# Kernel optimization log

Hardware: AMD Instinct MI355X
Metric: run time of the kernel (lower is better)

The kernel has to match this reference:

```python
import jax, jax.numpy as jnp
import numpy as np

BETA = 0.25  # commitment weight per level (vqconfig default)
EPS = 1e-12  # F.normalize eps


def setup_inputs() -> dict:
    key = jax.random.key(0)
    k1, k2 = jax.random.split(key)
    z = jax.random.normal(k1, (4, 256, 32, 32), dtype=jnp.float32)
    cb = jax.random.normal(k2, (4, 4096, 256), dtype=jnp.float32)
    # embeddings are row-normalized at init in the torch module
    cb = cb / jnp.maximum(jnp.linalg.norm(cb, axis=-1, keepdims=True), EPS)
    return {"z": z, "codebooks": cb}


def _nearest_code(r_flat, embed):
    """use_znorm=True path: cosine-similarity nearest neighbor.
    r_flat: (N, C), embed: (K, C) -> idx: (N,) int32"""
    rn = r_flat / jnp.maximum(jnp.linalg.norm(r_flat, axis=1, keepdims=True), EPS)
    en = embed / jnp.maximum(jnp.linalg.norm(embed, axis=1, keepdims=True), EPS)
    sim = jnp.einsum('nc,kc->nk', rn, en)  # (N, K)
    return jnp.argmax(sim, axis=1)


def reference(z, codebooks):
    """Residual VQ over L codebooks (eval mode: no EMA / kmeans init).
    z: (B, C, H, W); codebooks: (L, K, C).
    Returns (z_q_st (B,C,H,W), indices (L,B,H,W), qloss scalar)."""
    B, C, H, W = z.shape
    L = codebooks.shape[0]
    z_flat = z.transpose(0, 2, 3, 1).reshape(-1, C)  # (N, C)
    residual = z_flat
    q_sum = jnp.zeros_like(z_flat)
    qloss = jnp.zeros((), dtype=z.dtype)
    indices = []
    for l in range(L):  # small fixed level loop with sequential data dependency
        E = codebooks[l]
        idx = _nearest_code(residual, E)          # (N,)
        z_q = E[idx]                              # gather (N, C)
        q_sum = q_sum + z_q
        qloss = qloss + BETA * jnp.mean((jax.lax.stop_gradient(z_q) - residual) ** 2)
        residual = residual - jax.lax.stop_gradient(z_q)
        indices.append(idx.reshape(B, H, W))
    q = q_sum.reshape(B, H, W, C).transpose(0, 3, 1, 2)
    z_q_st = z + jax.lax.stop_gradient(q - z)     # straight-through estimator
    return z_q_st, jnp.stack(indices, axis=0), qloss
```

## Files before the change

### kernel.cpp

```cpp
#include <hip/hip_runtime.h>


#define OFF_AS   0
#define OFF_BS   524288
#define OFF_R    2621440
#define OFF_INV  3670016
#define OFF_PV   3686400
#define OFF_RN   3817472
#define OFF_CNT  3821568
#define OFF_CAND 3825664
#define OFF_CVAL 4874240
#define OFF_SSQ  5922816

#define BETA 0.25f
#define EPSN 1e-12f
#define CAP 256
#define SLC 16
#define OVF (1 << 20)
#define MARGIN 0.012f
#define NEGINF -3.0e38f

typedef __attribute__((ext_vector_type(8))) short short8;
typedef __attribute__((ext_vector_type(4))) short short4v;
typedef __attribute__((ext_vector_type(4))) float f32x4;

__device__ __forceinline__ unsigned short f2bf(float x) {
  unsigned u = __float_as_uint(x);
  unsigned r = (u + 0x7fffu + ((u >> 16) & 1u)) >> 16;
  return (unsigned short)r;
}

__device__ __forceinline__ void gload16(const void* g, void* s) {
  __builtin_amdgcn_global_load_lds(
      (const __attribute__((address_space(1))) unsigned int*)g,
      (__attribute__((address_space(3))) unsigned int*)s, 16, 0, 0);
}

__global__ __launch_bounds__(256) void k_prep(const float* __restrict__ z,
                                              const float* __restrict__ cb,
                                              float* __restrict__ r,
                                              unsigned short* __restrict__ AS,
                                              float* __restrict__ rnorm,
                                              int* __restrict__ cnt,
                                              float* __restrict__ inv,
                                              unsigned short* __restrict__ BS) {
  __shared__ __align__(16) char psm[9472];
  int tid = threadIdx.x;
  int w = tid >> 6, lane = tid & 63;
  if (blockIdx.x < 2048) {
    float (*t)[260] = (float(*)[260])psm;
    float* sinvs = (float*)(psm + 8320);
    int r0 = blockIdx.x * 8;
#pragma unroll
    for (int p = 0; p < 2; ++p) {
      int idx = p * 1024 + tid * 4;
      float4 v = *(const float4*)(cb + (size_t)r0 * 256 + idx);
      int row = idx >> 8, c = idx & 255;
      *(float4*)&t[row][c] = v;
    }
    __syncthreads();
#pragma unroll
    for (int rr = 0; rr < 2; ++rr) {
      int row = w * 2 + rr;
      float4 v = *(const float4*)&t[row][lane * 4];
      float s = v.x * v.x + v.y * v.y + v.z * v.z + v.w * v.w;
#pragma unroll
      for (int off = 32; off; off >>= 1) s += __shfl_xor(s, off);
      if (lane == 0) sinvs[row] = 1.0f / fmaxf(sqrtf(s), EPSN);
    }
    __syncthreads();
    if (tid < 8) inv[r0 + tid] = sinvs[tid];
#pragma unroll
    for (int p = 0; p < 2; ++p) {
      int idx = p * 1024 + tid * 4;
      int row = idx >> 8, c = idx & 255;
      float sc = sinvs[row];
      short4v s4;
      s4[0] = (short)f2bf(t[row][c + 0] * sc);
      s4[1] = (short)f2bf(t[row][c + 1] * sc);
      s4[2] = (short)f2bf(t[row][c + 2] * sc);
      s4[3] = (short)f2bf(t[row][c + 3] * sc);
      *(short4v*)(BS + (size_t)r0 * 256 + idx) = s4;
    }
  } else {
    float (*t)[9] = (float(*)[9])psm;
    float* wpart = (float*)(psm + 9216);
    int n0 = (blockIdx.x - 2048) * 8;
    int b = n0 >> 10, hw0 = n0 & 1023;
#pragma unroll
    for (int p = 0; p < 8; ++p) {
      int c = p * 32 + (tid >> 3), h = tid & 7;
      t[c][h] = z[((b * 256 + c) << 10) + hw0 + h];
    }
    __syncthreads();
#pragma unroll
    for (int h = 0; h < 8; ++h) {
      float v = t[tid][h];
      float s = v * v;
#pragma unroll
      for (int off = 32; off; off >>= 1) s += __shfl_xor(s, off);
      if (lane == 0) wpart[w * 8 + h] = s;
    }
    __syncthreads();
    if (tid < 8) {
      float tot = (wpart[0 * 8 + tid] + wpart[1 * 8 + tid]) +
                  (wpart[2 * 8 + tid] + wpart[3 * 8 + tid]);
      rnorm[n0 + tid] = sqrtf(tot);
      cnt[n0 + tid] = 0;
    }
#pragma unroll
    for (int h = 0; h < 8; ++h) {
      float v = t[tid][h];
      r[(n0 + h) * 256 + tid] = v;
      AS[(n0 + h) * 256 + tid] = f2bf(v);
    }
  }
}

__global__ __launch_bounds__(256) void k_gemm_argmax(
    const unsigned short* __restrict__ AS, const unsigned short* __restrict__ BS,
    float* __restrict__ pval, const float* __restrict__ rnorm,
    int* __restrict__ cnt, int* __restrict__ cand, float* __restrict__ cval) {
  __shared__ __align__(16) char sm[32768];
  unsigned short* lA = (unsigned short*)sm;
  unsigned short* lB = (unsigned short*)(sm + 16384);
  float* sv    = (float*)sm;
  float* scomb = (float*)(sm + 1024);
  float* rn_s  = (float*)(sm + 1536);
  int*   lcnt  = (int*)(sm + 2048);
  int*   lck   = (int*)(sm + 2560);
  float* lcv   = (float*)(sm + 10752);

  int bid = blockIdx.x;
  int wg = (bid & 7) * 128 + (bid >> 3);
  int bm = wg >> 5, bn = wg & 31;
  int mbase = bm * 128, nbase = bn * 128;
  int tid = threadIdx.x;
  int wid = tid >> 6, ln = tid & 63;
  int wr = wid >> 1, wc = wid & 1;
  int grp = ln >> 4, li = ln & 15;

  f32x4 acc[4][4];
#pragma unroll
  for (int i = 0; i < 4; ++i)
#pragma unroll
    for (int j = 0; j < 4; ++j) acc[i][j] = (f32x4){0.f, 0.f, 0.f, 0.f};

  for (int ks = 0; ks < 4; ++ks) {
    __syncthreads();
    int k0 = ks * 64;
#pragma unroll
    for (int i = 0; i < 4; ++i) {
      int idx = i * 256 + tid;
      int row = idx >> 3, cc = idx & 7;
      int src = cc ^ (row & 7);
      gload16(AS + ((mbase + row) << 8) + k0 + src * 8, ((char*)lA) + idx * 16);
    }
#pragma unroll
    for (int i = 0; i < 4; ++i) {
      int idx = i * 256 + tid;
      int row = idx >> 3, cc = idx & 7;
      int src = cc ^ (row & 7);
      gload16(BS + ((nbase + row) << 8) + k0 + src * 8, ((char*)lB) + idx * 16);
    }
    __syncthreads();
#pragma unroll
    for (int kk = 0; kk < 2; ++kk) {
      short8 b[4];
#pragma unroll
      for (int ni = 0; ni < 4; ++ni) {
        int row = wc * 64 + ni * 16 + li;
        int cc = kk * 4 + grp;
        b[ni] = *(const short8*)(((const char*)lB) + row * 128 + (cc ^ (row & 7)) * 16);
      }
#pragma unroll
      for (int mi = 0; mi < 4; ++mi) {
        int row = wr * 64 + mi * 16 + li;
        int cc = kk * 4 + grp;
        short8 a = *(const short8*)(((const char*)lA) + row * 128 + (cc ^ (row & 7)) * 16);
#pragma unroll
        for (int ni = 0; ni < 4; ++ni)
          acc[mi][ni] = __builtin_amdgcn_mfma_f32_16x16x32_bf16(a, b[ni], acc[mi][ni], 0, 0, 0);
      }
    }
  }

  float redv[4][4];
#pragma unroll
  for (int mi = 0; mi < 4; ++mi) {
#pragma unroll
    for (int reg = 0; reg < 4; ++reg) {
      float v = acc[mi][0][reg];
#pragma unroll
      for (int ni = 1; ni < 4; ++ni) v = fmaxf(v, acc[mi][ni][reg]);
#pragma unroll
      for (int off = 1; off < 16; off <<= 1) v = fmaxf(v, __shfl_xor(v, off));
      redv[mi][reg] = v;
    }
  }
  __syncthreads();
#pragma unroll
  for (int mi = 0; mi < 4; ++mi)
#pragma unroll
    for (int reg = 0; reg < 4; ++reg)
      if (li == 0) sv[(wr * 2 + wc) * 64 + mi * 16 + grp * 4 + reg] = redv[mi][reg];
  __syncthreads();
  if (tid < 128) {
    int wr2 = tid >> 6, r64 = tid & 63;
    float m = fmaxf(sv[(wr2 * 2 + 0) * 64 + r64], sv[(wr2 * 2 + 1) * 64 + r64]);
    int n = mbase + wr2 * 64 + r64;
    pval[n * 32 + bn] = m;
    scomb[wr2 * 64 + r64] = m;
    rn_s[wr2 * 64 + r64] = rnorm[n];
    lcnt[tid] = 0;
  }
  __syncthreads();
#pragma unroll
  for (int mi = 0; mi < 4; ++mi) {
#pragma unroll
    for (int reg = 0; reg < 4; ++reg) {
      int rl = mi * 16 + grp * 4 + reg;
      float thr = scomb[wr * 64 + rl] - MARGIN * rn_s[wr * 64 + rl];
      int rloc = wr * 64 + rl;
#pragma unroll
      for (int ni = 0; ni < 4; ++ni) {
        float v = acc[mi][ni][reg];
        if (v >= thr) {
          int pos = atomicAdd(&lcnt[rloc], 1);
          if (pos < SLC) {
            lck[rloc * SLC + pos] = nbase + wc * 64 + ni * 16 + li;
            lcv[rloc * SLC + pos] = v;
          }
        }
      }
    }
  }
  __syncthreads();
  if (tid < 128) {
    int rloc = tid;
    int n = mbase + rloc;
    int raw = lcnt[rloc];
    int lc = raw < SLC ? raw : SLC;
    int add = raw > SLC ? (lc + OVF) : lc;
    if (add > 0) {
      int base = atomicAdd(&cnt[n], add);
      for (int j = 0; j < lc; ++j) {
        int pos = base + j;
        if (pos < CAP) {
          cand[n * CAP + pos] = lck[rloc * SLC + j];
          cval[n * CAP + pos] = lcv[rloc * SLC + j];
        }
      }
    }
  }
}

__global__ __launch_bounds__(256) void k_refine_update(
    const float* __restrict__ cb, const float* __restrict__ inv,
    float* __restrict__ r, const float* __restrict__ pval,
    float* __restrict__ rnorm, int* __restrict__ cnt,
    const int* __restrict__ cand, const float* __restrict__ cval,
    unsigned short* __restrict__ AS, float* __restrict__ ssq,
    float* __restrict__ out_idx, int l) {
  __shared__ float rrow[256];
  __shared__ float gm_s;
  __shared__ int list[CAP];
  __shared__ int lcnt;
  __shared__ float wbv[4];
  __shared__ int wbk[4];
  __shared__ int sbk;
  __shared__ float wsum[4];

  int n = blockIdx.x, tid = threadIdx.x;
  int w = tid >> 6, lane = tid & 63;
  rrow[tid] = r[(n << 8) + tid];
  if (tid == 0) lcnt = 0;
  if (tid < 64) {
    float v = (lane < 32) ? pval[n * 32 + lane] : NEGINF;
#pragma unroll
    for (int off = 1; off < 32; off <<= 1) v = fmaxf(v, __shfl_xor(v, off));
    if (tid == 0) gm_s = v;
  }
  __syncthreads();

  int c = cnt[n];
  const float* cbl = cb + ((size_t)l << 20);
  const float* invl = inv + (l << 12);
  float bv = NEGINF; int bk = 0x7fffffff;
  float4 rv4 = *(const float4*)(rrow + lane * 4);

  if (c <= CAP) {
    float thr = gm_s - MARGIN * rnorm[n];
    if (tid < c) {
      float v = cval[n * CAP + tid];
      if (v >= thr) { int p = atomicAdd(&lcnt, 1); list[p] = cand[n * CAP + tid]; }
    }
    __syncthreads();
    int m = lcnt;
    for (int j = w; j < m; j += 4) {
      int k = list[j];
      float4 e4 = *(const float4*)(cbl + ((size_t)k << 8) + lane * 4);
      float p = rv4.x * e4.x + rv4.y * e4.y + rv4.z * e4.z + rv4.w * e4.w;
#pragma unroll
      for (int off = 32; off; off >>= 1) p += __shfl_xor(p, off);
      float s = p * invl[k];
      if (s > bv || (s == bv && k < bk)) { bv = s; bk = k; }
    }
  } else {
    __syncthreads();
    for (int kk = 0; kk < 1024; ++kk) {
      int k = kk * 4 + w;
      float4 e4 = *(const float4*)(cbl + ((size_t)k << 8) + lane * 4);
      float p = rv4.x * e4.x + rv4.y * e4.y + rv4.z * e4.z + rv4.w * e4.w;
#pragma unroll
      for (int off = 32; off; off >>= 1) p += __shfl_xor(p, off);
      float s = p * invl[k];
      if (s > bv || (s == bv && k < bk)) { bv = s; bk = k; }
    }
  }
  if (lane == 0) { wbv[w] = bv; wbk[w] = bk; }
  __syncthreads();
  if (tid == 0) {
    float v0 = wbv[0]; int i0 = wbk[0];
#pragma unroll
    for (int ww = 1; ww < 4; ++ww) {
      float ov = wbv[ww]; int oi = wbk[ww];
      if (ov > v0 || (ov == v0 && oi < i0)) { v0 = ov; i0 = oi; }
    }
    sbk = i0;
    out_idx[(l << 12) + n] = (float)i0;
  }
  __syncthreads();

  int ii = sbk;
  float e = cbl[((size_t)ii << 8) + tid];
  float rvv = rrow[tid] - e;
  r[(n << 8) + tid] = rvv;
  AS[(n << 8) + tid] = f2bf(rvv);
  float sq = rvv * rvv;
#pragma unroll
  for (int off = 32; off; off >>= 1) sq += __shfl_xor(sq, off);
  if (lane == 0) wsum[w] = sq;
  __syncthreads();
  if (tid == 0) {
    float tot = (wsum[0] + wsum[1]) + (wsum[2] + wsum[3]);
    ssq[(l << 12) + n] = tot;
    rnorm[n] = sqrtf(tot);
    cnt[n] = 0;
  }
}

__global__ __launch_bounds__(256) void k_writeq_qloss(const float* __restrict__ z,
                                                      const float* __restrict__ r,
                                                      const float* __restrict__ ssq,
                                                      float* __restrict__ out) {
  int tid = threadIdx.x;
  if (blockIdx.x == 1024) {
    __shared__ float wsumq[4];
    float q = 0.f;
    for (int l = 0; l < 4; ++l) {
      float p = 0.f;
#pragma unroll
      for (int i = 0; i < 16; ++i) p += ssq[l * 4096 + i * 256 + tid];
      int lane = tid & 63, w = tid >> 6;
#pragma unroll
      for (int off = 32; off; off >>= 1) p += __shfl_xor(p, off);
      if (lane == 0) wsumq[w] = p;
      __syncthreads();
      float tot = (wsumq[0] + wsumq[1]) + (wsumq[2] + wsumq[3]);
      q += BETA * (tot * (1.0f / (4096.0f * 256.0f)));
      __syncthreads();
    }
    if (tid == 0) out[1048576 + 16384] = q;
    return;
  }
  __shared__ float t[32][33];
  int id = blockIdx.x;
  int b = id >> 8; int rem = id & 255; int ct = rem >> 5; int ht = rem & 31;
  int c0 = ct * 32, h0 = ht * 32;
  int col = tid & 31, row0 = tid >> 5;
#pragma unroll
  for (int p = 0; p < 4; ++p) {
    int row = row0 + p * 8;
    t[row][col] = r[(b * 1024 + h0 + row) * 256 + c0 + col];
  }
  __syncthreads();
#pragma unroll
  for (int p = 0; p < 4; ++p) {
    int row = row0 + p * 8;
    int o = ((b * 256 + c0 + row) << 10) + h0 + col;
    out[o] = z[o] - t[col][row];
  }
}

extern "C" void kernel_launch(void* const* d_in, const int* in_sizes, int n_in,
                              void* d_out, int out_size, void* d_ws, size_t ws_size,
                              hipStream_t stream) {
  const float* z  = (const float*)d_in[0];
  const float* cb = (const float*)d_in[1];
  float* out = (float*)d_out;
  float* ws  = (float*)d_ws;

  unsigned short* AS = (unsigned short*)(ws + OFF_AS);
  unsigned short* BS = (unsigned short*)(ws + OFF_BS);
  float* r     = ws + OFF_R;
  float* inv   = ws + OFF_INV;
  float* pval  = ws + OFF_PV;
  float* rnorm = ws + OFF_RN;
  int*   cnt   = (int*)(ws + OFF_CNT);
  int*   cand  = (int*)(ws + OFF_CAND);
  float* cval  = ws + OFF_CVAL;
  float* ssq   = ws + OFF_SSQ;

  k_prep<<<2560, 256, 0, stream>>>(z, cb, r, AS, rnorm, cnt, inv, BS);
  for (int l = 0; l < 4; ++l) {
    k_gemm_argmax<<<1024, 256, 0, stream>>>(AS, BS + (size_t)l * 4096 * 256,
                                            pval, rnorm, cnt, cand, cval);
    k_refine_update<<<4096, 256, 0, stream>>>(cb, inv, r, pval, rnorm, cnt,
                                              cand, cval, AS, ssq,
                                              out + 1048576, l);
  }
  k_writeq_qloss<<<1025, 256, 0, stream>>>(z, r, ssq, out);
}
```

Baseline: 166.2 us.

## Widen GEMM-argmax tile to 128x256 and skip last-level residual side writes

The similarity GEMM tile grows from 128x128 to 128x256 codes per block, with two B buffers and two accumulator sets. This halves the grid to 512 blocks and halves the number of per-row partial maxima that refine must reduce, so each A tile is reused across twice as many codes. The cost is higher register and LDS use (48KB), which lowers occupancy, and only 512 blocks remain to fill the GPU. The final level also skips writing the bf16 residual, rnorm and counter reset, since nothing reads them afterward.

Result: slower. 198.9 us (+19.6%).

```diff
diff --git a/kernel.cpp b/kernel.cpp
--- a/kernel.cpp
+++ b/kernel.cpp
@@ -121,9 +121,10 @@
     const unsigned short* __restrict__ AS, const unsigned short* __restrict__ BS,
     float* __restrict__ pval, const float* __restrict__ rnorm,
     int* __restrict__ cnt, int* __restrict__ cand, float* __restrict__ cval) {
-  __shared__ __align__(16) char sm[32768];
-  unsigned short* lA = (unsigned short*)sm;
-  unsigned short* lB = (unsigned short*)(sm + 16384);
+  __shared__ __align__(16) char sm[49152];
+  unsigned short* lA  = (unsigned short*)sm;
+  unsigned short* lB0 = (unsigned short*)(sm + 16384);
+  unsigned short* lB1 = (unsigned short*)(sm + 32768);
   float* sv    = (float*)sm;
   float* scomb = (float*)(sm + 1024);
   float* rn_s  = (float*)(sm + 1536);
@@ -132,19 +133,22 @@
   float* lcv   = (float*)(sm + 10752);
 
   int bid = blockIdx.x;
-  int wg = (bid & 7) * 128 + (bid >> 3);
-  int bm = wg >> 5, bn = wg & 31;
-  int mbase = bm * 128, nbase = bn * 128;
+  int wg = (bid & 7) * 64 + (bid >> 3);
+  int bm = wg >> 4, bn = wg & 15;
+  int mbase = bm * 128, nbase = bn * 256;
   int tid = threadIdx.x;
   int wid = tid >> 6, ln = tid & 63;
   int wr = wid >> 1, wc = wid & 1;
   int grp = ln >> 4, li = ln & 15;
 
-  f32x4 acc[4][4];
+  f32x4 acc0[4][4], acc1[4][4];
 #pragma unroll
   for (int i = 0; i < 4; ++i)
 #pragma unroll
-    for (int j = 0; j < 4; ++j) acc[i][j] = (f32x4){0.f, 0.f, 0.f, 0.f};
+    for (int j = 0; j < 4; ++j) {
+      acc0[i][j] = (f32x4){0.f, 0.f, 0.f, 0.f};
+      acc1[i][j] = (f32x4){0.f, 0.f, 0.f, 0.f};
+    }
 
   for (int ks = 0; ks < 4; ++ks) {
     __syncthreads();
@@ -161,17 +165,26 @@
       int idx = i * 256 + tid;
       int row = idx >> 3, cc = idx & 7;
       int src = cc ^ (row & 7);
-      gload16(BS + ((nbase + row) << 8) + k0 + src * 8, ((char*)lB) + idx * 16);
+      gload16(BS + ((nbase + row) << 8) + k0 + src * 8, ((char*)lB0) + idx * 16);
+    }
+#pragma unroll
+    for (int i = 0; i < 4; ++i) {
+      int idx = i * 256 + tid;
+      int row = idx >> 3, cc = idx & 7;
+      int src = cc ^ (row & 7);
+      gload16(BS + ((nbase + 128 + row) << 8) + k0 + src * 8, ((char*)lB1) + idx * 16);
     }
     __syncthreads();
 #pragma unroll
     for (int kk = 0; kk < 2; ++kk) {
-      short8 b[4];
+      short8 b0[4], b1[4];
 #pragma unroll
       for (int ni = 0; ni < 4; ++ni) {
         int row = wc * 64 + ni * 16 + li;
         int cc = kk * 4 + grp;
-        b[ni] = *(const short8*)(((const char*)lB) + row * 128 + (cc ^ (row & 7)) * 16);
+        int off = row * 128 + (cc ^ (row & 7)) * 16;
+        b0[ni] = *(const short8*)(((const char*)lB0) + off);
+        b1[ni] = *(const short8*)(((const char*)lB1) + off);
       }
 #pragma unroll
       for (int mi = 0; mi < 4; ++mi) {
@@ -179,8 +192,10 @@
         int cc = kk * 4 + grp;
         short8 a = *(const short8*)(((const char*)lA) + row * 128 + (cc ^ (row & 7)) * 16);
 #pragma unroll
-        for (int ni = 0; ni < 4; ++ni)
-          acc[mi][ni] = __builtin_amdgcn_mfma_f32_16x16x32_bf16(a, b[ni], acc[mi][ni], 0, 0, 0);
+        for (int ni = 0; ni < 4; ++ni) {
+          acc0[mi][ni] = __builtin_amdgcn_mfma_f32_16x16x32_bf16(a, b0[ni], acc0[mi][ni], 0, 0, 0);
+          acc1[mi][ni] = __builtin_amdgcn_mfma_f32_16x16x32_bf16(a, b1[ni], acc1[mi][ni], 0, 0, 0);
+        }
       }
     }
   }
@@ -190,9 +205,10 @@
   for (int mi = 0; mi < 4; ++mi) {
 #pragma unroll
     for (int reg = 0; reg < 4; ++reg) {
-      float v = acc[mi][0][reg];
-#pragma unroll
-      for (int ni = 1; ni < 4; ++ni) v = fmaxf(v, acc[mi][ni][reg]);
+      float v = fmaxf(acc0[mi][0][reg], acc1[mi][0][reg]);
+#pragma unroll
+      for (int ni = 1; ni < 4; ++ni)
+        v = fmaxf(v, fmaxf(acc0[mi][ni][reg], acc1[mi][ni][reg]));
 #pragma unroll
       for (int off = 1; off < 16; off <<= 1) v = fmaxf(v, __shfl_xor(v, off));
       redv[mi][reg] = v;
@@ -209,7 +225,7 @@
     int wr2 = tid >> 6, r64 = tid & 63;
     float m = fmaxf(sv[(wr2 * 2 + 0) * 64 + r64], sv[(wr2 * 2 + 1) * 64 + r64]);
     int n = mbase + wr2 * 64 + r64;
-    pval[n * 32 + bn] = m;
+    pval[n * 16 + bn] = m;
     scomb[wr2 * 64 + r64] = m;
     rn_s[wr2 * 64 + r64] = rnorm[n];
     lcnt[tid] = 0;
@@ -224,12 +240,20 @@
       int rloc = wr * 64 + rl;
 #pragma unroll
       for (int ni = 0; ni < 4; ++ni) {
-        float v = acc[mi][ni][reg];
-        if (v >= thr) {
+        float v0 = acc0[mi][ni][reg];
+        if (v0 >= thr) {
           int pos = atomicAdd(&lcnt[rloc], 1);
           if (pos < SLC) {
             lck[rloc * SLC + pos] = nbase + wc * 64 + ni * 16 + li;
-            lcv[rloc * SLC + pos] = v;
+            lcv[rloc * SLC + pos] = v0;
+          }
+        }
+        float v1 = acc1[mi][ni][reg];
+        if (v1 >= thr) {
+          int pos = atomicAdd(&lcnt[rloc], 1);
+          if (pos < SLC) {
+            lck[rloc * SLC + pos] = nbase + 128 + wc * 64 + ni * 16 + li;
+            lcv[rloc * SLC + pos] = v1;
           }
         }
       }
@@ -276,9 +300,9 @@
   rrow[tid] = r[(n << 8) + tid];
   if (tid == 0) lcnt = 0;
   if (tid < 64) {
-    float v = (lane < 32) ? pval[n * 32 + lane] : NEGINF;
-#pragma unroll
-    for (int off = 1; off < 32; off <<= 1) v = fmaxf(v, __shfl_xor(v, off));
+    float v = (lane < 16) ? pval[n * 16 + lane] : NEGINF;
+#pragma unroll
+    for (int off = 1; off < 16; off <<= 1) v = fmaxf(v, __shfl_xor(v, off));
     if (tid == 0) gm_s = v;
   }
   __syncthreads();
@@ -336,7 +360,7 @@
   float e = cbl[((size_t)ii << 8) + tid];
   float rvv = rrow[tid] - e;
   r[(n << 8) + tid] = rvv;
-  AS[(n << 8) + tid] = f2bf(rvv);
+  if (l != 3) AS[(n << 8) + tid] = f2bf(rvv);
   float sq = rvv * rvv;
 #pragma unroll
   for (int off = 32; off; off >>= 1) sq += __shfl_xor(sq, off);
@@ -345,8 +369,7 @@
   if (tid == 0) {
     float tot = (wsum[0] + wsum[1]) + (wsum[2] + wsum[3]);
     ssq[(l << 12) + n] = tot;
-    rnorm[n] = sqrtf(tot);
-    cnt[n] = 0;
+    if (l != 3) { rnorm[n] = sqrtf(tot); cnt[n] = 0; }
   }
 }
 
@@ -414,8 +437,8 @@
 
   k_prep<<<2560, 256, 0, stream>>>(z, cb, r, AS, rnorm, cnt, inv, BS);
   for (int l = 0; l < 4; ++l) {
-    k_gemm_argmax<<<1024, 256, 0, stream>>>(AS, BS + (size_t)l * 4096 * 256,
-                                            pval, rnorm, cnt, cand, cval);
+    k_gemm_argmax<<<512, 256, 0, stream>>>(AS, BS + (size_t)l * 4096 * 256,
+                                           pval, rnorm, cnt, cand, cval);
     k_refine_update<<<4096, 256, 0, stream>>>(cb, inv, r, pval, rnorm, cnt,
                                               cand, cval, AS, ssq,
                                               out + 1048576, l);
```

## Map one wavefront per row in refine kernel, drop block syncs

Applied to the files above, without the earlier changes.

The refine/update kernel now gives each 64-lane wavefront its own residual row, four rows per block, instead of one row per 256-thread block. Candidate filtering, rescoring, argmax, residual update and norm computation all run inside a single wavefront using shuffles and a per-wave shared list, so block-wide barriers and the cross-wave argmax merge disappear. It also vectorizes the residual and bf16 stores and skips the AS, rnorm and cnt writes on the last level. The cost is that each wave rescores its candidates serially, and the overflow fallback scans all 4096 codes in one wave, which is slower when it triggers.

Measured after the change: 164.6 us. No clear change (-1.0%).

```diff
diff --git a/kernel.cpp b/kernel.cpp
--- a/kernel.cpp
+++ b/kernel.cpp
@@ -262,43 +262,35 @@
     const int* __restrict__ cand, const float* __restrict__ cval,
     unsigned short* __restrict__ AS, float* __restrict__ ssq,
     float* __restrict__ out_idx, int l) {
-  __shared__ float rrow[256];
-  __shared__ float gm_s;
-  __shared__ int list[CAP];
-  __shared__ int lcnt;
-  __shared__ float wbv[4];
-  __shared__ int wbk[4];
-  __shared__ int sbk;
-  __shared__ float wsum[4];
-
-  int n = blockIdx.x, tid = threadIdx.x;
-  int w = tid >> 6, lane = tid & 63;
-  rrow[tid] = r[(n << 8) + tid];
-  if (tid == 0) lcnt = 0;
-  if (tid < 64) {
-    float v = (lane < 32) ? pval[n * 32 + lane] : NEGINF;
-#pragma unroll
-    for (int off = 1; off < 32; off <<= 1) v = fmaxf(v, __shfl_xor(v, off));
-    if (tid == 0) gm_s = v;
-  }
-  __syncthreads();
-
-  int c = cnt[n];
+  __shared__ int lists[4][CAP];
+  __shared__ int lcnts[4];
+  int tid = threadIdx.x, w = tid >> 6, lane = tid & 63;
+  int n = blockIdx.x * 4 + w;
   const float* cbl = cb + ((size_t)l << 20);
   const float* invl = inv + (l << 12);
+
+  float4 rv4 = *(const float4*)(r + ((size_t)n << 8) + lane * 4);
+
+  float v = (lane < 32) ? pval[n * 32 + lane] : NEGINF;
+#pragma unroll
+  for (int off = 16; off; off >>= 1) v = fmaxf(v, __shfl_xor(v, off));
+  float gm = __shfl(v, 0);
+
+  if (lane == 0) lcnts[w] = 0;
+  int c = cnt[n];
   float bv = NEGINF; int bk = 0x7fffffff;
-  float4 rv4 = *(const float4*)(rrow + lane * 4);
 
   if (c <= CAP) {
-    float thr = gm_s - MARGIN * rnorm[n];
-    if (tid < c) {
-      float v = cval[n * CAP + tid];
-      if (v >= thr) { int p = atomicAdd(&lcnt, 1); list[p] = cand[n * CAP + tid]; }
-    }
-    __syncthreads();
-    int m = lcnt;
-    for (int j = w; j < m; j += 4) {
-      int k = list[j];
+    float thr = gm - MARGIN * rnorm[n];
+    for (int j = lane; j < c; j += 64) {
+      if (cval[n * CAP + j] >= thr) {
+        int p = atomicAdd(&lcnts[w], 1);
+        lists[w][p] = cand[n * CAP + j];
+      }
+    }
+    int m = lcnts[w];
+    for (int j = 0; j < m; ++j) {
+      int k = lists[w][j];
       float4 e4 = *(const float4*)(cbl + ((size_t)k << 8) + lane * 4);
       float p = rv4.x * e4.x + rv4.y * e4.y + rv4.z * e4.z + rv4.w * e4.w;
 #pragma unroll
@@ -307,9 +299,7 @@
       if (s > bv || (s == bv && k < bk)) { bv = s; bk = k; }
     }
   } else {
-    __syncthreads();
-    for (int kk = 0; kk < 1024; ++kk) {
-      int k = kk * 4 + w;
+    for (int k = 0; k < 4096; ++k) {
       float4 e4 = *(const float4*)(cbl + ((size_t)k << 8) + lane * 4);
       float p = rv4.x * e4.x + rv4.y * e4.y + rv4.z * e4.z + rv4.w * e4.w;
 #pragma unroll
@@ -318,35 +308,23 @@
       if (s > bv || (s == bv && k < bk)) { bv = s; bk = k; }
     }
   }
-  if (lane == 0) { wbv[w] = bv; wbk[w] = bk; }
-  __syncthreads();
-  if (tid == 0) {
-    float v0 = wbv[0]; int i0 = wbk[0];
-#pragma unroll
-    for (int ww = 1; ww < 4; ++ww) {
-      float ov = wbv[ww]; int oi = wbk[ww];
-      if (ov > v0 || (ov == v0 && oi < i0)) { v0 = ov; i0 = oi; }
-    }
-    sbk = i0;
-    out_idx[(l << 12) + n] = (float)i0;
-  }
-  __syncthreads();
-
-  int ii = sbk;
-  float e = cbl[((size_t)ii << 8) + tid];
-  float rvv = rrow[tid] - e;
-  r[(n << 8) + tid] = rvv;
-  AS[(n << 8) + tid] = f2bf(rvv);
-  float sq = rvv * rvv;
+  if (lane == 0) out_idx[(l << 12) + n] = (float)bk;
+
+  float4 e4 = *(const float4*)(cbl + ((size_t)bk << 8) + lane * 4);
+  float4 nv = {rv4.x - e4.x, rv4.y - e4.y, rv4.z - e4.z, rv4.w - e4.w};
+  *(float4*)(r + ((size_t)n << 8) + lane * 4) = nv;
+  if (l != 3) {
+    short4v s4;
+    s4[0] = (short)f2bf(nv.x); s4[1] = (short)f2bf(nv.y);
+    s4[2] = (short)f2bf(nv.z); s4[3] = (short)f2bf(nv.w);
+    *(short4v*)(AS + ((size_t)n << 8) + lane * 4) = s4;
+  }
+  float sq = nv.x * nv.x + nv.y * nv.y + nv.z * nv.z + nv.w * nv.w;
 #pragma unroll
   for (int off = 32; off; off >>= 1) sq += __shfl_xor(sq, off);
-  if (lane == 0) wsum[w] = sq;
-  __syncthreads();
-  if (tid == 0) {
-    float tot = (wsum[0] + wsum[1]) + (wsum[2] + wsum[3]);
-    ssq[(l << 12) + n] = tot;
-    rnorm[n] = sqrtf(tot);
-    cnt[n] = 0;
+  if (lane == 0) {
+    ssq[(l << 12) + n] = sq;
+    if (l != 3) { rnorm[n] = sqrtf(sq); cnt[n] = 0; }
   }
 }
 
@@ -416,7 +394,7 @@
   for (int l = 0; l < 4; ++l) {
     k_gemm_argmax<<<1024, 256, 0, stream>>>(AS, BS + (size_t)l * 4096 * 256,
                                             pval, rnorm, cnt, cand, cval);
-    k_refine_update<<<4096, 256, 0, stream>>>(cb, inv, r, pval, rnorm, cnt,
+    k_refine_update<<<1024, 256, 0, stream>>>(cb, inv, r, pval, rnorm, cnt,
                                               cand, cval, AS, ssq,
                                               out + 1048576, l);
   }
```
